# Kernel tuning notes

Hardware: AMD Instinct MI355X
Metric: run time of the kernel (lower is better)

Reference implementation:

```python
import jax, jax.numpy as jnp
import numpy as np

B, E, K, HD = 128, 1024, 64, 256


def setup_inputs() -> dict:
    key = jax.random.key(0)
    ks = jax.random.split(key, 9)
    std = 0.01
    ev = jax.random.randint(ks[0], (B, E), 0, K)
    seq = jax.nn.one_hot(ev, K, dtype=jnp.float32)
    lengths = jax.random.randint(ks[1], (B,), E // 2, E + 1)
    mask = jnp.arange(E)[None, :] < lengths[:, None]  # prefix (ragged) mask
    dts = jax.random.uniform(ks[2], (B, E + 1), minval=0.01, maxval=1.0)
    times = jnp.cumsum(dts, axis=1).astype(jnp.float32)  # increasing, [B, E+1]
    U_w = jax.random.normal(ks[3], (7 * HD, K), dtype=jnp.float32) * std
    U_b = jax.random.normal(ks[4], (7 * HD,), dtype=jnp.float32) * std
    V_w = jax.random.normal(ks[5], (7 * HD, HD), dtype=jnp.float32) * std
    V_b = jax.random.normal(ks[6], (7 * HD,), dtype=jnp.float32) * std
    Lw = jax.random.normal(ks[7], (K, HD), dtype=jnp.float32) * std  # L_lamb_til weight
    scale = jnp.ones((K,), dtype=jnp.float32)
    return {"seq": seq, "mask": mask, "times": times, "U_w": U_w, "U_b": U_b,
            "V_w": V_w, "V_b": V_b, "Lw": Lw, "scale": scale}


def reference(seq, mask, times, U_w, U_b, V_w, V_b, Lw, scale):
    Nb, Ne, Kk = seq.shape
    hD = V_w.shape[1]
    sig = jax.nn.sigmoid

    def step(carry, inp):
        ct, cbar, ht = carry
        x, m, tnow, tnext = inp  # [B,K], [B], [B], [B]
        nn = x @ U_w.T + U_b + ht @ V_w.T + V_b  # [B, 7*hD]
        ih, fh, ibh, fbh, zh, oh, dh = jnp.split(nn, 7, axis=1)
        i, f = sig(ih), sig(fh)
        iBar, fBar = sig(ibh), sig(fbh)
        z, o = 2.0 * sig(zh), sig(oh)
        delta = jax.nn.softplus(dh)
        clow = f * ct + i * z
        cbar_new = fBar * cbar + iBar * z
        dt = (tnext - tnow)[:, None]
        ct_new = cbar_new + (clow - cbar_new) * jnp.exp(-dt * delta)
        ht_new = o * (2.0 * sig(2.0 * ct_new) - 1.0)
        lamb_til = ht_new @ Lw.T  # [B, K]
        lamb = scale * jnp.log1p(jnp.exp(lamb_til / scale))
        mm = m[:, None]
        ct2 = jnp.where(mm, ct_new, ct)
        cbar2 = jnp.where(mm, cbar_new, cbar)
        ht2 = jnp.where(mm, ht_new, ht)
        z0 = jnp.zeros((), seq.dtype)
        outs = (jnp.where(mm, lamb, z0), jnp.where(mm, clow, z0),
                jnp.where(mm, cbar_new, z0), jnp.where(mm, delta, z0),
                jnp.where(mm, o, z0))
        return (ct2, cbar2, ht2), outs

    init = (jnp.zeros((Nb, hD), seq.dtype),
            jnp.zeros((Nb, hD), seq.dtype),
            jnp.zeros((Nb, hD), seq.dtype))
    xs = (seq.swapaxes(0, 1), mask.T, times[:, :Ne].T, times[:, 1:Ne + 1].T)
    _, (lambOuts, CLows, Cbars, deltas, OutGates) = jax.lax.scan(step, init, xs)
    # scan stacks along event dim first -> move back to [B, E, *]
    return (lambOuts.swapaxes(0, 1), CLows.swapaxes(0, 1), Cbars.swapaxes(0, 1),
            deltas.swapaxes(0, 1), OutGates.swapaxes(0, 1))
```

## Files before the change

kernel.cpp:

```cpp
#include <hip/hip_runtime.h>
#include <stdint.h>

#define Bn  128
#define En  1024
#define Kn  64
#define HDn 256
#define NGc 8
#define NSc 16

typedef short s8v __attribute__((ext_vector_type(8)));
typedef float f4v __attribute__((ext_vector_type(4)));

static __device__ __forceinline__ unsigned short f2bf(float f) {
  union { float f; unsigned u; } cv; cv.f = f;
  unsigned u = cv.u;
  unsigned r = u + 0x7fffu + ((u >> 16) & 1u);
  return (unsigned short)(r >> 16);
}
static __device__ __forceinline__ float sigm(float x) {
  return 1.0f / (1.0f + __expf(-x));
}

__global__ void detect_mask_fmt(const uint8_t* __restrict__ m8, int* __restrict__ fmt) {
  const int b = blockIdx.x;
  const int e0 = threadIdx.x * 4;
  const uint8_t* row = m8 + (size_t)b * En;
  int bad = 0;
  uint8_t prev = row[e0];
  #pragma unroll
  for (int i = 1; i <= 4; ++i) {
    int e = e0 + i;
    if (e < En) {
      uint8_t cur = row[e];
      if (prev == 0 && cur != 0) bad = 1;
      prev = cur;
    }
  }
  if (threadIdx.x == 0 && row[0] == 0) bad = 1;
  if (bad) atomicOr(fmt, 1);
}

__global__ void compute_ev(const float* __restrict__ seq, int* __restrict__ ev) {
  const int idx  = blockIdx.x * 4 + (threadIdx.x >> 6);
  const int lane = threadIdx.x & 63;
  float v = seq[(size_t)idx * Kn + lane];
  unsigned long long m = __ballot(v > 0.5f);
  if (lane == 0) ev[idx] = __ffsll((long long)m) - 1;
}

__global__ __launch_bounds__(64, 1) void ct_main(
    const float* __restrict__ times, const uint8_t* __restrict__ mask8,
    const float* __restrict__ U_w,  const float* __restrict__ U_b,
    const float* __restrict__ V_w,  const float* __restrict__ V_b,
    const float* __restrict__ Lw,   const float* __restrict__ scale,
    const int* __restrict__ ev,     unsigned short* __restrict__ h_buf,
    int* __restrict__ ctr,          const int* __restrict__ fmtp,
    float* __restrict__ out_lam, float* __restrict__ out_cl,
    float* __restrict__ out_cb,  float* __restrict__ out_dl,
    float* __restrict__ out_og)
{
  __shared__ float U_lds[64 * 16 * 12];

  const int lane = threadIdx.x;
  const int col  = lane & 15;
  const int quad = lane >> 4;
  const int g    = blockIdx.x >> 4;
  const int s    = blockIdx.x & 15;
  const int d0   = s * 16;
  const int fmt  = *fmtp;

  #pragma unroll 1
  for (int i = lane; i < 64 * 16 * 12; i += 64) U_lds[i] = 0.0f;
  #pragma unroll 1
  for (int i = lane; i < 7 * 16 * 64; i += 64) {
    int k = i & 63, dl = (i >> 6) & 15, g7 = i >> 10;
    U_lds[(k * 16 + dl) * 12 + g7] = U_w[(size_t)(g7 * HDn + d0 + dl) * Kn + k];
  }
  __syncthreads();

  s8v Bv[7][8];
  #pragma unroll
  for (int g7 = 0; g7 < 7; ++g7) {
    const float* src = V_w + (size_t)(g7 * HDn + d0 + col) * HDn;
    #pragma unroll
    for (int kc = 0; kc < 8; ++kc) {
      const float* p = src + kc * 32 + quad * 8;
      f4v a = *(const f4v*)(p);
      f4v b = *(const f4v*)(p + 4);
      s8v fr;
      fr[0] = (short)f2bf(a[0]); fr[1] = (short)f2bf(a[1]);
      fr[2] = (short)f2bf(a[2]); fr[3] = (short)f2bf(a[3]);
      fr[4] = (short)f2bf(b[0]); fr[5] = (short)f2bf(b[1]);
      fr[6] = (short)f2bf(b[2]); fr[7] = (short)f2bf(b[3]);
      Bv[g7][kc] = fr;
    }
  }
  s8v BL[8];
  const int kkc = s * 4 + col;
  {
    const bool lv = (col < 4);
    const float* src = Lw + (size_t)(lv ? kkc : 0) * HDn;
    #pragma unroll
    for (int kc = 0; kc < 8; ++kc) {
      const float* p = src + kc * 32 + quad * 8;
      s8v fr;
      #pragma unroll
      for (int j = 0; j < 8; ++j) fr[j] = lv ? (short)f2bf(p[j]) : (short)0;
      BL[kc] = fr;
    }
  }
  float bias[7];
  #pragma unroll
  for (int g7 = 0; g7 < 7; ++g7) {
    int j = g7 * HDn + d0 + col;
    bias[g7] = U_b[j] + V_b[j];
  }
  const float sc = scale[(kkc < Kn) ? kkc : 0];

  unsigned int* hbuf32 = (unsigned int*)h_buf;

  float c[4]  = {0, 0, 0, 0}, cb[4] = {0, 0, 0, 0};
  float hreg[4] = {0, 0, 0, 0}, pm[4] = {0, 0, 0, 0};
  int* my_ctr = ctr + g * 32;

  #pragma unroll 1
  for (int t = 0; t <= En; ++t) {
    const bool has_main = (t < En);

    int evv[4]; float dtv[4], mk[4];
    f4v u0v[4], u1v[4];
    if (has_main) {
      #pragma unroll
      for (int r = 0; r < 4; ++r) {
        const int bglob = g * 16 + quad * 4 + r;
        evv[r] = ev[(size_t)bglob * En + t];
        const float* tp = times + (size_t)bglob * (En + 1) + t;
        dtv[r] = tp[1] - tp[0];
        int mraw;
        if (fmt) mraw = ((const int*)mask8)[(size_t)bglob * En + t];
        else     mraw = (int)mask8[(size_t)bglob * En + t];
        mk[r] = (mraw != 0) ? 1.0f : 0.0f;
      }
      #pragma unroll
      for (int r = 0; r < 4; ++r) {
        const float* up = U_lds + ((size_t)evv[r] * 16 + col) * 12;
        u0v[r] = *(const f4v*)(up);
        u1v[r] = *(const f4v*)(up + 4);
      }
    }

    float pmo[4];
    #pragma unroll
    for (int r = 0; r < 4; ++r) pmo[r] = pm[r];

    if (t > 0) {
      const int target = NSc * t;
      if (lane == 0) {
        while (__hip_atomic_load(my_ctr, __ATOMIC_RELAXED,
                                 __HIP_MEMORY_SCOPE_AGENT) < target) {
          __builtin_amdgcn_s_sleep(1);
        }
      }
      __builtin_amdgcn_sched_barrier(0);
      asm volatile("" ::: "memory");
    }

    const int par = t & 1;
    const unsigned int* hb32 = hbuf32 + (size_t)(par * NGc + g) * 2048;
    s8v A[8];
    #pragma unroll
    for (int kc = 0; kc < 8; ++kc) {
      const int base = (kc * 2 + (quad >> 1)) * 128 + col * 8 + (quad & 1) * 4;
      union { unsigned int u[4]; s8v v; } cvt;
      #pragma unroll
      for (int j = 0; j < 4; ++j)
        cvt.u[j] = __hip_atomic_load(hb32 + base + j, __ATOMIC_RELAXED,
                                     __HIP_MEMORY_SCOPE_AGENT);
      A[kc] = cvt.v;
    }

    f4v acc[7] = {}; f4v accL = {0.0f, 0.0f, 0.0f, 0.0f};
    if (has_main) {
      #pragma unroll
      for (int kc = 0; kc < 8; ++kc) {
        #pragma unroll
        for (int g7 = 0; g7 < 7; ++g7)
          acc[g7] = __builtin_amdgcn_mfma_f32_16x16x32_bf16(A[kc], Bv[g7][kc], acc[g7], 0, 0, 0);
      }
    }
    #pragma unroll
    for (int kc = 0; kc < 8; ++kc)
      accL = __builtin_amdgcn_mfma_f32_16x16x32_bf16(A[kc], BL[kc], accL, 0, 0, 0);

    float clv[4], cbv[4], dlv[4], ogv[4];
    if (has_main) {
      #pragma unroll
      for (int r = 0; r < 4; ++r) {
        float nn0 = acc[0][r] + u0v[r][0] + bias[0];
        float nn1 = acc[1][r] + u0v[r][1] + bias[1];
        float nn2 = acc[2][r] + u0v[r][2] + bias[2];
        float nn3 = acc[3][r] + u0v[r][3] + bias[3];
        float nn4 = acc[4][r] + u1v[r][0] + bias[4];
        float nn5 = acc[5][r] + u1v[r][1] + bias[5];
        float nn6 = acc[6][r] + u1v[r][2] + bias[6];
        float i_ = sigm(nn0), f_ = sigm(nn1);
        float ib = sigm(nn2), fb = sigm(nn3);
        float z_ = 2.0f * sigm(nn4), o_ = sigm(nn5);
        float dl = __logf(1.0f + __expf(nn6));
        float clow = f_ * c[r] + i_ * z_;
        float cbn  = fb * cb[r] + ib * z_;
        float ed   = __expf(-dtv[r] * dl);
        float cn   = cbn + (clow - cbn) * ed;
        float hn   = o_ * (2.0f * sigm(2.0f * cn) - 1.0f);
        const bool mb = (mk[r] != 0.0f);
        c[r]    = mb ? cn  : c[r];
        cb[r]   = mb ? cbn : cb[r];
        hreg[r] = mb ? hn  : hreg[r];
        pm[r]   = mk[r];
        clv[r] = mb ? clow : 0.0f;
        cbv[r] = mb ? cbn  : 0.0f;
        dlv[r] = mb ? dl   : 0.0f;
        ogv[r] = mb ? o_   : 0.0f;
      }

      const int par2 = (t + 1) & 1;
      unsigned int* hw32 = hbuf32 + (size_t)(par2 * NGc + g) * 2048 + s * 128;
      float hsw[4];
      #pragma unroll
      for (int r = 0; r < 4; ++r) hsw[r] = __shfl_xor(hreg[r], 1, 64);
      const int evn = (col & 1);
      unsigned int w[4];
      #pragma unroll
      for (int r = 0; r < 4; ++r) {
        unsigned int a  = f2bf(hreg[r]);
        unsigned int bn = f2bf(hsw[r]);
        w[r] = evn ? (bn | (a << 16)) : (a | (bn << 16));
      }
      const unsigned int wa = evn ? w[2] : w[0];
      const unsigned int wb = evn ? w[3] : w[1];
      const int ra = evn ? 2 : 0;
      __hip_atomic_store(hw32 + (quad * 4 + ra) * 8 + (col >> 1), wa,
                         __ATOMIC_RELAXED, __HIP_MEMORY_SCOPE_AGENT);
      __hip_atomic_store(hw32 + (quad * 4 + ra + 1) * 8 + (col >> 1), wb,
                         __ATOMIC_RELAXED, __HIP_MEMORY_SCOPE_AGENT);
      asm volatile("s_waitcnt vmcnt(0)" ::: "memory");
      if (lane == 0)
        __hip_atomic_fetch_add(my_ctr, 1, __ATOMIC_RELAXED,
                               __HIP_MEMORY_SCOPE_AGENT);
    }

    if (t > 0 && col < 4) {
      #pragma unroll
      for (int r = 0; r < 4; ++r) {
        const int bglob = g * 16 + quad * 4 + r;
        float q   = accL[r] / sc;
        float lam = sc * __logf(1.0f + __expf(q));
        __builtin_nontemporal_store((pmo[r] != 0.0f) ? lam : 0.0f,
            &out_lam[((size_t)bglob * En + (t - 1)) * Kn + kkc]);
      }
    }

    if (has_main) {
      #pragma unroll
      for (int r = 0; r < 4; ++r) {
        const size_t off =
            ((size_t)(g * 16 + quad * 4 + r) * En + t) * HDn + d0 + col;
        __builtin_nontemporal_store(clv[r], &out_cl[off]);
        __builtin_nontemporal_store(cbv[r], &out_cb[off]);
        __builtin_nontemporal_store(dlv[r], &out_dl[off]);
        __builtin_nontemporal_store(ogv[r], &out_og[off]);
      }
    }
  }
}

extern "C" void kernel_launch(void* const* d_in, const int* in_sizes, int n_in,
                              void* d_out, int out_size, void* d_ws, size_t ws_size,
                              hipStream_t stream) {
  const float*   seq   = (const float*)d_in[0];
  const uint8_t* mask  = (const uint8_t*)d_in[1];
  const float*   times = (const float*)d_in[2];
  const float*   U_w   = (const float*)d_in[3];
  const float*   U_b   = (const float*)d_in[4];
  const float*   V_w   = (const float*)d_in[5];
  const float*   V_b   = (const float*)d_in[6];
  const float*   Lw    = (const float*)d_in[7];
  const float*   scale = (const float*)d_in[8];

  char* ws = (char*)d_ws;
  unsigned short* h_buf = (unsigned short*)ws;
  int* ctr = (int*)(ws + 131072);
  int* fmt = (int*)(ws + 132096);
  int* ev  = (int*)(ws + 132224);

  hipMemsetAsync(d_ws, 0, 132224, stream);

  detect_mask_fmt<<<dim3(Bn), dim3(256), 0, stream>>>(mask, fmt);
  compute_ev<<<dim3(Bn * En / 4), dim3(256), 0, stream>>>(seq, ev);

  float* out = (float*)d_out;
  float* out_lam = out;
  float* out_cl  = out_lam + (size_t)Bn * En * Kn;
  float* out_cb  = out_cl  + (size_t)Bn * En * HDn;
  float* out_dl  = out_cb  + (size_t)Bn * En * HDn;
  float* out_og  = out_dl  + (size_t)Bn * En * HDn;

  ct_main<<<dim3(NGc * NSc), dim3(64), 0, stream>>>(
      times, mask, U_w, U_b, V_w, V_b, Lw, scale,
      ev, h_buf, ctr, fmt, out_lam, out_cl, out_cb, out_dl, out_og);
}
```

Baseline: 5.553 ms.

## Group four slice waves per block, share local h via LDS, flag-based peer sync

Restructures the persistent recurrent kernel from 128 single-wave blocks into 32 blocks of four waves. The four waves in a block exchange their quarter of the hidden state through LDS, and only the other three quarters are read from global memory. The single atomic counter per batch group becomes per-block step flags, and each block polls its three peer blocks. The U_w gather table moves from LDS to a global pre-transposed layout built by a new small kernel. This is meant to cut global traffic and sync latency on the serial per-timestep path, at the cost of an intra-block __syncthreads every step and uncached global reads for the U gather.

```diff
diff --git a/kernel.cpp b/kernel.cpp
--- a/kernel.cpp
+++ b/kernel.cpp
@@ -6,7 +6,8 @@
 #define Kn  64
 #define HDn 256
 #define NGc 8
-#define NSc 16
+#define NHc 4
+#define NWc 4
 
 typedef short s8v __attribute__((ext_vector_type(8)));
 typedef float f4v __attribute__((ext_vector_type(4)));
@@ -48,9 +49,19 @@
   if (lane == 0) ev[idx] = __ffsll((long long)m) - 1;
 }
 
-__global__ __launch_bounds__(64, 1) void ct_main(
+__global__ void make_ut(const float* __restrict__ U_w, float* __restrict__ Ut) {
+  const int k = blockIdx.x;
+  const int j = threadIdx.x;
+  float* dst = Ut + ((size_t)k * HDn + j) * 8;
+  #pragma unroll
+  for (int g7 = 0; g7 < 7; ++g7)
+    dst[g7] = U_w[((size_t)g7 * HDn + j) * Kn + k];
+  dst[7] = 0.0f;
+}
+
+__global__ __launch_bounds__(256, 1) void ct_main(
     const float* __restrict__ times, const uint8_t* __restrict__ mask8,
-    const float* __restrict__ U_w,  const float* __restrict__ U_b,
+    const float* __restrict__ Ut,   const float* __restrict__ U_b,
     const float* __restrict__ V_w,  const float* __restrict__ V_b,
     const float* __restrict__ Lw,   const float* __restrict__ scale,
     const int* __restrict__ ev,     unsigned short* __restrict__ h_buf,
@@ -59,23 +70,20 @@
     float* __restrict__ out_cb,  float* __restrict__ out_dl,
     float* __restrict__ out_og)
 {
-  __shared__ float U_lds[64 * 16 * 12];
-
-  const int lane = threadIdx.x;
+  __shared__ unsigned short h_lds[2][16 * 64];
+
+  const int tid  = threadIdx.x;
+  const int lane = tid & 63;
+  const int wv   = tid >> 6;
   const int col  = lane & 15;
   const int quad = lane >> 4;
-  const int g    = blockIdx.x >> 4;
-  const int s    = blockIdx.x & 15;
+  const int g    = blockIdx.x & 7;
+  const int hh   = blockIdx.x >> 3;
+  const int s    = hh * NWc + wv;
   const int d0   = s * 16;
   const int fmt  = *fmtp;
 
-  #pragma unroll 1
-  for (int i = lane; i < 64 * 16 * 12; i += 64) U_lds[i] = 0.0f;
-  #pragma unroll 1
-  for (int i = lane; i < 7 * 16 * 64; i += 64) {
-    int k = i & 63, dl = (i >> 6) & 15, g7 = i >> 10;
-    U_lds[(k * 16 + dl) * 12 + g7] = U_w[(size_t)(g7 * HDn + d0 + dl) * Kn + k];
-  }
+  for (int i = tid; i < 2 * 16 * 64; i += 256) h_lds[0][i] = 0;
   __syncthreads();
 
   s8v Bv[7][8];
@@ -119,9 +127,14 @@
 
   unsigned int* hbuf32 = (unsigned int*)h_buf;
 
+  int* flag_my = ctr + (hh * 8 + g) * 32;
+  int* flag_p0 = ctr + ((((hh + 1) & 3) * 8) + g) * 32;
+  int* flag_p1 = ctr + ((((hh + 2) & 3) * 8) + g) * 32;
+  int* flag_p2 = ctr + ((((hh + 3) & 3) * 8) + g) * 32;
+  int p0 = 0, p1 = 0, p2 = 0;
+
   float c[4]  = {0, 0, 0, 0}, cb[4] = {0, 0, 0, 0};
   float hreg[4] = {0, 0, 0, 0}, pm[4] = {0, 0, 0, 0};
-  int* my_ctr = ctr + g * 32;
 
   #pragma unroll 1
   for (int t = 0; t <= En; ++t) {
@@ -143,7 +156,7 @@
       }
       #pragma unroll
       for (int r = 0; r < 4; ++r) {
-        const float* up = U_lds + ((size_t)evv[r] * 16 + col) * 12;
+        const float* up = Ut + ((size_t)evv[r] * HDn + d0 + col) * 8;
         u0v[r] = *(const f4v*)(up);
         u1v[r] = *(const f4v*)(up + 4);
       }
@@ -154,10 +167,12 @@
     for (int r = 0; r < 4; ++r) pmo[r] = pm[r];
 
     if (t > 0) {
-      const int target = NSc * t;
-      if (lane == 0) {
-        while (__hip_atomic_load(my_ctr, __ATOMIC_RELAXED,
-                                 __HIP_MEMORY_SCOPE_AGENT) < target) {
+      if (p0 < t || p1 < t || p2 < t) {
+        for (;;) {
+          p0 = __hip_atomic_load(flag_p0, __ATOMIC_RELAXED, __HIP_MEMORY_SCOPE_AGENT);
+          p1 = __hip_atomic_load(flag_p1, __ATOMIC_RELAXED, __HIP_MEMORY_SCOPE_AGENT);
+          p2 = __hip_atomic_load(flag_p2, __ATOMIC_RELAXED, __HIP_MEMORY_SCOPE_AGENT);
+          if (p0 >= t && p1 >= t && p2 >= t) break;
           __builtin_amdgcn_s_sleep(1);
         }
       }
@@ -166,17 +181,29 @@
     }
 
     const int par = t & 1;
-    const unsigned int* hb32 = hbuf32 + (size_t)(par * NGc + g) * 2048;
+    const unsigned long long* hb64 =
+        (const unsigned long long*)(h_buf + (size_t)(par * NGc + g) * 4096);
+    const char* lbase_r = (const char*)&h_lds[par][0];
     s8v A[8];
     #pragma unroll
     for (int kc = 0; kc < 8; ++kc) {
-      const int base = (kc * 2 + (quad >> 1)) * 128 + col * 8 + (quad & 1) * 4;
-      union { unsigned int u[4]; s8v v; } cvt;
-      #pragma unroll
-      for (int j = 0; j < 4; ++j)
-        cvt.u[j] = __hip_atomic_load(hb32 + base + j, __ATOMIC_RELAXED,
-                                     __HIP_MEMORY_SCOPE_AGENT);
-      A[kc] = cvt.v;
+      if ((kc >> 1) != hh) {
+        const int sp = kc * 2 + (quad >> 1);
+        const unsigned long long* q = hb64 + sp * 64 + col * 4 + (quad & 1) * 2;
+        union { unsigned long long q[2]; s8v v; } u;
+        u.q[0] = __hip_atomic_load(q + 0, __ATOMIC_RELAXED, __HIP_MEMORY_SCOPE_AGENT);
+        u.q[1] = __hip_atomic_load(q + 1, __ATOMIC_RELAXED, __HIP_MEMORY_SCOPE_AGENT);
+        A[kc] = u.v;
+      }
+    }
+    #pragma unroll
+    for (int kc = 0; kc < 8; ++kc) {
+      if ((kc >> 1) == hh) {
+        const int kcl = kc & 1;
+        const unsigned boff =
+            (unsigned)(col * 128 + kcl * 64 + quad * 16) ^ ((unsigned)(col & 7) << 4);
+        A[kc] = *(const s8v*)(lbase_r + boff);
+      }
     }
 
     f4v acc[7] = {}; f4v accL = {0.0f, 0.0f, 0.0f, 0.0f};
@@ -224,7 +251,6 @@
       }
 
       const int par2 = (t + 1) & 1;
-      unsigned int* hw32 = hbuf32 + (size_t)(par2 * NGc + g) * 2048 + s * 128;
       float hsw[4];
       #pragma unroll
       for (int r = 0; r < 4; ++r) hsw[r] = __shfl_xor(hreg[r], 1, 64);
@@ -238,15 +264,27 @@
       }
       const unsigned int wa = evn ? w[2] : w[0];
       const unsigned int wb = evn ? w[3] : w[1];
-      const int ra = evn ? 2 : 0;
-      __hip_atomic_store(hw32 + (quad * 4 + ra) * 8 + (col >> 1), wa,
+      const int ra    = evn ? 2 : 0;
+      const int row_a = quad * 4 + ra;
+      const int row_b = row_a + 1;
+      char* lbase_w = (char*)&h_lds[par2][0];
+      const unsigned xa =
+          (unsigned)(row_a * 128 + (wv * 16 + (col & ~1)) * 2) ^ ((unsigned)(row_a & 7) << 4);
+      const unsigned xb =
+          (unsigned)(row_b * 128 + (wv * 16 + (col & ~1)) * 2) ^ ((unsigned)(row_b & 7) << 4);
+      *(unsigned int*)(lbase_w + xa) = wa;
+      *(unsigned int*)(lbase_w + xb) = wb;
+      unsigned int* hw32 = hbuf32 + (size_t)(par2 * NGc + g) * 2048 + s * 128;
+      __hip_atomic_store(hw32 + row_a * 8 + (col >> 1), wa,
                          __ATOMIC_RELAXED, __HIP_MEMORY_SCOPE_AGENT);
-      __hip_atomic_store(hw32 + (quad * 4 + ra + 1) * 8 + (col >> 1), wb,
+      __hip_atomic_store(hw32 + row_b * 8 + (col >> 1), wb,
                          __ATOMIC_RELAXED, __HIP_MEMORY_SCOPE_AGENT);
-      asm volatile("s_waitcnt vmcnt(0)" ::: "memory");
-      if (lane == 0)
-        __hip_atomic_fetch_add(my_ctr, 1, __ATOMIC_RELAXED,
-                               __HIP_MEMORY_SCOPE_AGENT);
+      __syncthreads();
+      if (tid == 0)
+        __hip_atomic_store(flag_my, t + 1, __ATOMIC_RELAXED, __HIP_MEMORY_SCOPE_AGENT);
+      p0 = __hip_atomic_load(flag_p0, __ATOMIC_RELAXED, __HIP_MEMORY_SCOPE_AGENT);
+      p1 = __hip_atomic_load(flag_p1, __ATOMIC_RELAXED, __HIP_MEMORY_SCOPE_AGENT);
+      p2 = __hip_atomic_load(flag_p2, __ATOMIC_RELAXED, __HIP_MEMORY_SCOPE_AGENT);
     }
 
     if (t > 0 && col < 4) {
@@ -289,14 +327,16 @@
 
   char* ws = (char*)d_ws;
   unsigned short* h_buf = (unsigned short*)ws;
-  int* ctr = (int*)(ws + 131072);
-  int* fmt = (int*)(ws + 132096);
-  int* ev  = (int*)(ws + 132224);
-
-  hipMemsetAsync(d_ws, 0, 132224, stream);
+  int* ctr  = (int*)(ws + 131072);
+  int* fmt  = (int*)(ws + 135168);
+  float* Ut = (float*)(ws + 135296);
+  int* ev   = (int*)(ws + 659584);
+
+  hipMemsetAsync(d_ws, 0, 135296, stream);
 
   detect_mask_fmt<<<dim3(Bn), dim3(256), 0, stream>>>(mask, fmt);
   compute_ev<<<dim3(Bn * En / 4), dim3(256), 0, stream>>>(seq, ev);
+  make_ut<<<dim3(Kn), dim3(HDn), 0, stream>>>(U_w, Ut);
 
   float* out = (float*)d_out;
   float* out_lam = out;
@@ -305,7 +345,7 @@
   float* out_dl  = out_cb  + (size_t)Bn * En * HDn;
   float* out_og  = out_dl  + (size_t)Bn * En * HDn;
 
-  ct_main<<<dim3(NGc * NSc), dim3(64), 0, stream>>>(
-      times, mask, U_w, U_b, V_w, V_b, Lw, scale,
+  ct_main<<<dim3(NGc * NHc), dim3(64 * NWc), 0, stream>>>(
+      times, mask, Ut, U_b, V_w, V_b, Lw, scale,
       ev, h_buf, ctr, fmt, out_lam, out_cl, out_cb, out_dl, out_og);
 }
```

After: 6.243 ms. 12.4% more time.
